# Kernel tuning notes

Measured on AMD Instinct MI355X. Metric: run time of the kernel, lower is better.

The kernel has to match this reference:

```python
import jax, jax.numpy as jnp
import numpy as np

B, S, D = 2, 2048, 1024
H, HD = 16, 64
FF = 4096
LOCAL_W, RAND_P = 256, 0.2
EPS = 1e-5
NEG = -9e15


def _linear_params(key, din, dout):
    kw, kb = jax.random.split(key)
    bound = 1.0 / np.sqrt(din)
    W = jax.random.uniform(kw, (din, dout), jnp.float32, -bound, bound)
    b = jax.random.uniform(kb, (dout,), jnp.float32, -bound, bound)
    return W, b


def setup_inputs() -> dict:
    key = jax.random.key(0)
    ks = jax.random.split(key, 10)
    x = jax.random.normal(ks[0], (B, S, D), jnp.float32)
    # local + random mask, as in create_local_mask
    i = np.arange(S)[:, None]
    j = np.arange(S)[None, :]
    local = (np.abs(i - j) <= LOCAL_W // 2)
    rnd = np.asarray(jax.random.bernoulli(ks[1], RAND_P, (S, S)))
    mask = jnp.asarray(np.logical_or(local, rnd).astype(np.int32))
    Wq, bq = _linear_params(ks[2], D, D)
    Wk, bk = _linear_params(ks[3], D, D)
    Wv, bv = _linear_params(ks[4], D, D)
    Wo, bo = _linear_params(ks[5], D, D)
    W1, b1 = _linear_params(ks[6], D, FF)
    W2, b2 = _linear_params(ks[7], FF, D)
    g1 = jnp.ones((D,), jnp.float32); be1 = jnp.zeros((D,), jnp.float32)
    g2 = jnp.ones((D,), jnp.float32); be2 = jnp.zeros((D,), jnp.float32)
    return dict(x=x, mask=mask, Wq=Wq, bq=bq, Wk=Wk, bk=bk, Wv=Wv, bv=bv,
                Wo=Wo, bo=bo, W1=W1, b1=b1, W2=W2, b2=b2,
                g1=g1, be1=be1, g2=g2, be2=be2)


def _layernorm(x, g, b):
    mu = jnp.mean(x, axis=-1, keepdims=True)
    var = jnp.mean(jnp.square(x - mu), axis=-1, keepdims=True)
    return (x - mu) * jax.lax.rsqrt(var + EPS) * g + b


def reference(x, mask, Wq, bq, Wk, bk, Wv, bv, Wo, bo, W1, b1, W2, b2, g1, be1, g2, be2):
    scale = jnp.float32(np.sqrt(HD))  # sqrt(head_dim), requires_grad=False
    q = x @ Wq + bq
    k = x @ Wk + bk
    v = x @ Wv + bv
    # faithful to original: view(B, heads, S, head_dim) WITHOUT transpose
    q = q.reshape(B, H, S, HD)
    k = k.reshape(B, H, S, HD)
    v = v.reshape(B, H, S, HD)
    scores = jnp.einsum('bhsd,bhtd->bhst', q / scale, k)  # [B,H,S,S]
    scores = jnp.where(mask == 0, jnp.float32(NEG), scores)
    probs = jax.nn.softmax(scores, axis=-1)
    av = jnp.einsum('bhst,bhtd->bhsd', probs, v)
    # faithful reshape back: view(B, S, head_dim*heads)
    attn_out = av.reshape(B, S, H * HD) @ Wo + bo
    x = _layernorm(x + attn_out, g1, be1)
    ffn = jax.nn.gelu(x @ W1 + b1, approximate=False) @ W2 + b2
    x = _layernorm(x + ffn, g2, be2)
    return x
```

## Files before the change

kernel.cpp:

```cpp
#include <hip/hip_runtime.h>
#include <cstdint>
#include <cstddef>

namespace {

constexpr int kS  = 2048;
constexpr int kD  = 1024;
constexpr int kHD = 64;
constexpr int kTOK = 4096;

typedef float f32x4 __attribute__((ext_vector_type(4)));
typedef __bf16 bf16x8 __attribute__((ext_vector_type(8)));
typedef unsigned short u16x8 __attribute__((ext_vector_type(8)));

__device__ __forceinline__ unsigned short f2b(float f){
  unsigned int u = __builtin_bit_cast(unsigned int, f);
  u += 0x7fffu + ((u >> 16) & 1u);
  return (unsigned short)(u >> 16);
}

__device__ __forceinline__ float b2f(unsigned short u){
  return __builtin_bit_cast(float, (unsigned)u << 16);
}

__device__ __forceinline__ bf16x8 ldfrag(const unsigned short* p){
  return __builtin_bit_cast(bf16x8, *(const u16x8*)p);
}

__device__ __forceinline__ float fexp2(float x){
#if __has_builtin(__builtin_amdgcn_exp2f)
  return __builtin_amdgcn_exp2f(x);
#else
  return exp2f(x);
#endif
}

__device__ __forceinline__ void gl_lds16(const void* g, void* l){
  __builtin_amdgcn_global_load_lds(
      (__attribute__((address_space(1))) void*)(void*)g,
      (__attribute__((address_space(3))) void*)l, 16, 0, 0);
}

__device__ __forceinline__ bf16x8 ld_swz(const unsigned short* tile, int row, int slot){
  return ldfrag(tile + row * 64 + (((slot ^ row) & 7) << 3));
}

__device__ __forceinline__ void stageKt(const unsigned short* Kg, unsigned short* lds,
                                        int wave, int lane, int t0){
  #pragma unroll
  for (int i = 0; i < 2; ++i){
    const int lin = i * 4096 + wave * 1024 + lane * 16;
    const int r = lin >> 7;
    const int sl = (lin >> 4) & 7;
    const int sabs = t0 + r;
    gl_lds16(Kg + (size_t)(sabs >> 4) * 3072 + (sabs & 15) * 64 + (((sl ^ r) & 7) << 3),
             (char*)lds + i * 4096 + wave * 1024);
  }
}

__device__ __forceinline__ void stageVt(const unsigned short* Vh, unsigned short* lds,
                                        int wave, int lane, int t0){
  #pragma unroll
  for (int i = 0; i < 2; ++i){
    const int lin = i * 4096 + wave * 1024 + lane * 16;
    const int r = lin >> 7;
    const int sl = (lin >> 4) & 7;
    gl_lds16(Vh + (size_t)r * kS + t0 + (((sl ^ r) & 7) << 3),
             (char*)lds + i * 4096 + wave * 1024);
  }
}

__global__ __launch_bounds__(256) void cvt_bf16_kern(const float* __restrict__ X,
                                                     unsigned short* __restrict__ Y){
  int i = blockIdx.x * 256 + threadIdx.x;
  float4 v = ((const float4*)X)[i];
  ((ushort4*)Y)[i] = make_ushort4(f2b(v.x), f2b(v.y), f2b(v.z), f2b(v.w));
}

__global__ __launch_bounds__(256) void maskbits_kern(const int* __restrict__ mask,
                                                     unsigned long long* __restrict__ mb){
  const int gw   = (blockIdx.x * 256 + threadIdx.x) >> 6;
  const int lane = threadIdx.x & 63;
  const int row  = gw >> 5, word = gw & 31;
  const int key  = ((lane >> 2) & 3) * 16 + ((lane >> 4) & 3) * 4 + (lane & 3);
  const int m = mask[(size_t)row * kS + word * 64 + key];
  const unsigned long long b = __ballot(m != 0);
  if (lane == 0) mb[(size_t)row * 32 + word] = b;
}

__global__ __launch_bounds__(256) void catbias_kern(const float* __restrict__ a,
                                                    const float* __restrict__ b,
                                                    const float* __restrict__ c,
                                                    float* __restrict__ o){
  int i = blockIdx.x * 256 + threadIdx.x;
  float v = (i < 1024) ? a[i] : ((i < 2048) ? b[i - 1024] : c[i - 2048]);
  o[i] = v;
}

__global__ __launch_bounds__(256) void wtrans_kern(const float* __restrict__ W,
                                                   unsigned short* __restrict__ Wt,
                                                   int K, int N){
  __shared__ float t[32][33];
  int n0 = blockIdx.x * 32, k0 = blockIdx.y * 32;
  int tx = threadIdx.x & 31, ty = threadIdx.x >> 5;
  #pragma unroll
  for (int i = 0; i < 32; i += 8)
    t[ty + i][tx] = W[(size_t)(k0 + ty + i) * N + n0 + tx];
  __syncthreads();
  #pragma unroll
  for (int i = 0; i < 32; i += 8)
    Wt[(size_t)(n0 + ty + i) * K + k0 + tx] = f2b(t[tx][ty + i]);
}

__global__ __launch_bounds__(256) void vtrans_kern(const unsigned short* __restrict__ QKV,
                                                   unsigned short* __restrict__ Vt){
  __shared__ unsigned short t[64][65];
  int bh = blockIdx.y, s0 = blockIdx.x * 64;
  const int rowbase = (bh >> 4) * 2048 + (bh & 15) * 128;
  const unsigned short* Vg = QKV + (size_t)rowbase * 3072 + 2048;
  unsigned short* Vth = Vt + (size_t)bh * kHD * kS;
  int tx = threadIdx.x & 63, ty = threadIdx.x >> 6;
  #pragma unroll
  for (int i = 0; i < 64; i += 4){
    const int s = s0 + ty + i;
    t[ty + i][tx] = Vg[(size_t)(s >> 4) * 3072 + (s & 15) * 64 + tx];
  }
  __syncthreads();
  #pragma unroll
  for (int i = 0; i < 64; i += 4)
    Vth[(size_t)(ty + i) * kS + s0 + tx] = t[tx][ty + i];
}

template <int OUT_BF16, int ACT_GELU, int SPLITK>
__global__ __launch_bounds__(512, 2) void gemm256_kern(const unsigned short* __restrict__ A,
                                                       const unsigned short* __restrict__ Bt,
                                                       const float* __restrict__ bias,
                                                       void* __restrict__ C,
                                                       int M, int N, int K){
  __shared__ unsigned short As[2][2][128 * 64];
  __shared__ unsigned short Bs[2][2][128 * 64];
  int bid = blockIdx.y * gridDim.x + blockIdx.x;
  const int nwg = gridDim.x * gridDim.y;
  bid = (bid & 7) * (nwg >> 3) + (bid >> 3);
  const int bx = bid % gridDim.x, by = bid / gridDim.x;
  const int m0 = by << 8, n0 = bx << 8;
  const int tid  = threadIdx.x;
  const int wave = tid >> 6, lane = tid & 63;
  const int wr = wave >> 2, wc = wave & 3;
  const int lr = lane & 15, lk = lane >> 4;
  const int kz   = K / SPLITK;
  const int kbeg = (SPLITK > 1) ? blockIdx.z * kz : 0;
  const int NT   = kz >> 6;
  const int srow = tid >> 3;
  const int scol = ((tid & 7) ^ (srow & 7)) << 3;
  const unsigned short* Ag = A  + (size_t)(m0 + srow) * K + kbeg + scol;
  const unsigned short* Bg = Bt + (size_t)(n0 + srow) * K + kbeg + scol;
  const int dst = tid * 8;
  const int sk0 = ((    lk) ^ (lr & 7)) << 3;
  const int sk1 = ((4 + lk) ^ (lr & 7)) << 3;
  const int aro = lr * 64;
  const int bro = ((wc & 1) * 64 + lr) * 64;
  const int bh_ = wc >> 1;

  f32x4 acc[8][4] = {};
  bf16x8 aR[4][2], bR[2][2][2];

  auto stA = [&](int b, int h, int kt){
    const unsigned short* s = Ag + (size_t)(h * 128) * K + kt * 64;
    gl_lds16(s,                  &As[b][h][dst]);
    gl_lds16(s + (size_t)64 * K, &As[b][h][4096 + dst]);
  };
  auto stB = [&](int b, int h, int kt){
    const unsigned short* s = Bg + (size_t)(h * 128) * K + kt * 64;
    gl_lds16(s,                  &Bs[b][h][dst]);
    gl_lds16(s + (size_t)64 * K, &Bs[b][h][4096 + dst]);
  };

#define LOAD_A(b, MH) { \
  _Pragma("unroll") for (int mp = 0; mp < 4; ++mp){ \
    aR[mp][0] = ldfrag(&As[b][wr][aro + ((MH) * 64 + mp * 16) * 64 + sk0]); \
    aR[mp][1] = ldfrag(&As[b][wr][aro + ((MH) * 64 + mp * 16) * 64 + sk1]); } }
#define LOAD_B(b, NH) { \
  _Pragma("unroll") for (int np = 0; np < 2; ++np){ \
    bR[NH][np][0] = ldfrag(&Bs[b][bh_][bro + ((NH) * 32 + np * 16) * 64 + sk0]); \
    bR[NH][np][1] = ldfrag(&Bs[b][bh_][bro + ((NH) * 32 + np * 16) * 64 + sk1]); } }
#define QMFMA(MH, NH) { \
  _Pragma("unroll") for (int kk = 0; kk < 2; ++kk) \
  _Pragma("unroll") for (int mp = 0; mp < 4; ++mp) \
  _Pragma("unroll") for (int np = 0; np < 2; ++np) \
    acc[(MH)*4+mp][(NH)*2+np] = __builtin_amdgcn_mfma_f32_16x16x32_bf16( \
        aR[mp][kk], bR[NH][np][kk], acc[(MH)*4+mp][(NH)*2+np], 0, 0, 0); }
#define PHASE_TAIL(QM) \
  asm volatile("s_barrier" ::: "memory"); \
  asm volatile("s_waitcnt lgkmcnt(0)" ::: "memory"); \
  __builtin_amdgcn_sched_barrier(0); \
  __builtin_amdgcn_s_setprio(1); \
  QM; \
  __builtin_amdgcn_s_setprio(0); \
  __builtin_amdgcn_sched_barrier(0); \
  asm volatile("s_barrier" ::: "memory");

  stA(0, 0, 0); stB(0, 0, 0); stB(0, 1, 0); stA(0, 1, 0);
  asm volatile("s_waitcnt vmcnt(4)" ::: "memory");
  asm volatile("s_barrier" ::: "memory");

  for (int t = 0; t < NT; ++t){
    const int b = t & 1, bn = b ^ 1;
    const bool pf = (t + 1 < NT);
    LOAD_A(b, 0); LOAD_B(b, 0);
    if (pf){ stA(bn, 0, t + 1); asm volatile("s_waitcnt vmcnt(4)" ::: "memory"); }
    else   {                    asm volatile("s_waitcnt vmcnt(2)" ::: "memory"); }
    PHASE_TAIL(QMFMA(0, 0));
    LOAD_B(b, 1);
    if (pf){ stB(bn, 0, t + 1); asm volatile("s_waitcnt vmcnt(4)" ::: "memory"); }
    else   {                    asm volatile("s_waitcnt vmcnt(0)" ::: "memory"); }
    PHASE_TAIL(QMFMA(0, 1));
    LOAD_A(b, 1);
    if (pf){ stB(bn, 1, t + 1); }
    PHASE_TAIL(QMFMA(1, 0));
    if (pf){ stA(bn, 1, t + 1); asm volatile("s_waitcnt vmcnt(4)" ::: "memory"); }
    PHASE_TAIL(QMFMA(1, 1));
  }
#undef LOAD_A
#undef LOAD_B
#undef QMFMA
#undef PHASE_TAIL

  unsigned short* Cb = (unsigned short*)C + (SPLITK > 1 ? (size_t)blockIdx.z * M * N : 0);
  float*          Cf = (float*)C          + (SPLITK > 1 ? (size_t)blockIdx.z * M * N : 0);
  #pragma unroll
  for (int n = 0; n < 4; ++n){
    const int col = n0 + wc * 64 + n * 16 + lr;
    const float bv = (SPLITK == 1) ? bias[col] : 0.0f;
    #pragma unroll
    for (int m = 0; m < 8; ++m){
      #pragma unroll
      for (int j = 0; j < 4; ++j){
        const int row = m0 + wr * 128 + m * 16 + lk * 4 + j;
        float v = acc[m][n][j] + bv;
        if (ACT_GELU) v = 0.5f * v * (1.0f + erff(v * 0.70710678118654752f));
        if (OUT_BF16) Cb[(size_t)row * N + col] = f2b(v);
        else          Cf[(size_t)row * N + col] = v;
      }
    }
  }
}

__global__ __launch_bounds__(256) void attn_kern(const unsigned short* __restrict__ QKV,
                                                 const unsigned short* __restrict__ Vt,
                                                 const unsigned long long* __restrict__ mbits,
                                                 unsigned short* __restrict__ O){
  __shared__ unsigned short Ks[2][64 * 64];
  __shared__ unsigned short Vs[2][64 * 64];
  __shared__ unsigned short Ps[4][16 * 64];
  const int tid = threadIdx.x;
  const int wave = tid >> 6, lane = tid & 63;
  const int lr = lane & 15, lk = lane >> 4;
  const int bh = blockIdx.y;
  const int rowbase = (bh >> 4) * 2048 + (bh & 15) * 128;
  const unsigned short* Qg = QKV + (size_t)rowbase * 3072;
  const unsigned short* Kg = Qg + 1024;
  const unsigned short* Vh = Vt + (size_t)bh * kHD * kS;
  const int qbase = blockIdx.x * 64 + wave * 16;
  constexpr float kScl = 0.18033688011112042f;

  bf16x8 qf[2];
  { const int qr = qbase + lr;
    const unsigned short* qp = Qg + (size_t)(qr >> 4) * 3072 + (qr & 15) * 64 + lk * 8;
    qf[0] = ldfrag(qp); qf[1] = ldfrag(qp + 32); }

  f32x4 accO[4] = {};
  float lsum = 0.f;
  unsigned short* Pw = Ps[wave];
  char* Pwb = (char*)Pw + lr * 128 + ((lk & 1) << 3);
  const int lr7 = lr & 7;

  const unsigned long long* mrp = mbits + (size_t)(qbase + lr) * 32;
  unsigned long long mb = mrp[0];

  stageKt(Kg, Ks[0], wave, lane, 0);
  stageVt(Vh, Vs[0], wave, lane, 0);
  __syncthreads();

  int cur = 0;
  for (int t = 0; t < kS / 64; ++t){
    unsigned long long mbn = 0;
    if (t < kS / 64 - 1){
      stageKt(Kg, Ks[cur ^ 1], wave, lane, (t + 1) * 64);
      stageVt(Vh, Vs[cur ^ 1], wave, lane, (t + 1) * 64);
      mbn = mrp[t + 1];
    }
    f32x4 sa[4] = {};
    #pragma unroll
    for (int kk = 0; kk < 2; ++kk)
      #pragma unroll
      for (int n = 0; n < 4; ++n){
        bf16x8 kf = ld_swz(Ks[cur], n * 16 + lr, kk * 4 + lk);
        sa[n] = __builtin_amdgcn_mfma_f32_16x16x32_bf16(kf, qf[kk], sa[n], 0, 0, 0);
      }
    const unsigned wb = (unsigned)(mb >> (lk * 16));
    float s = 0.f;
    #pragma unroll
    for (int n = 0; n < 4; ++n){
      float p0, p1, p2, p3;
      {
        float v0 = fexp2(sa[n][0] * kScl), v1 = fexp2(sa[n][1] * kScl);
        float v2 = fexp2(sa[n][2] * kScl), v3 = fexp2(sa[n][3] * kScl);
        const int s0 = ((int)(wb << (31 - (n * 4 + 0)))) >> 31;
        const int s1 = ((int)(wb << (31 - (n * 4 + 1)))) >> 31;
        const int s2 = ((int)(wb << (31 - (n * 4 + 2)))) >> 31;
        const int s3 = ((int)(wb << (31 - (n * 4 + 3)))) >> 31;
        p0 = __builtin_bit_cast(float, __builtin_bit_cast(int, v0) & s0);
        p1 = __builtin_bit_cast(float, __builtin_bit_cast(int, v1) & s1);
        p2 = __builtin_bit_cast(float, __builtin_bit_cast(int, v2) & s2);
        p3 = __builtin_bit_cast(float, __builtin_bit_cast(int, v3) & s3);
      }
      s += (p0 + p1) + (p2 + p3);
      unsigned r0, r1;
      asm("v_cvt_pk_bf16_f32 %0, %1, %2" : "=v"(r0) : "v"(p0), "v"(p1));
      asm("v_cvt_pk_bf16_f32 %0, %1, %2" : "=v"(r1) : "v"(p2), "v"(p3));
      *(uint2*)(Pwb + (((2 * n + (lk >> 1)) ^ lr7) << 4)) = make_uint2(r0, r1);
    }
    s += __shfl_xor(s, 16);
    s += __shfl_xor(s, 32);
    lsum += s;
    #pragma unroll
    for (int kk = 0; kk < 2; ++kk){
      bf16x8 pf = ld_swz(Pw, lr, kk * 4 + lk);
      #pragma unroll
      for (int dd = 0; dd < 4; ++dd){
        bf16x8 vfr = ld_swz(Vs[cur], dd * 16 + lr, kk * 4 + lk);
        accO[dd] = __builtin_amdgcn_mfma_f32_16x16x32_bf16(pf, vfr, accO[dd], 0, 0, 0);
      }
    }
    mb = mbn;
    __syncthreads();
    cur ^= 1;
  }
  const size_t hoff = (size_t)bh * kS * kHD;
  #pragma unroll
  for (int j = 0; j < 4; ++j){
    const float inv = 1.0f / __shfl(lsum, lk * 4 + j);
    const int row = qbase + lk * 4 + j;
    #pragma unroll
    for (int dd = 0; dd < 4; ++dd)
      O[hoff + (size_t)row * 64 + dd * 16 + lr] = f2b(accO[dd][j] * inv);
  }
}

template <int NP, int PBF16, int OUT_B>
__global__ __launch_bounds__(256) void add_ln_kern(const float* __restrict__ X,
                                                   const void* __restrict__ P,
                                                   const float* __restrict__ bias,
                                                   const float* __restrict__ g,
                                                   const float* __restrict__ be,
                                                   float* __restrict__ Yf,
                                                   unsigned short* __restrict__ Yb){
  const int row = blockIdx.x;
  const int tid = threadIdx.x;
  const size_t pstride = (size_t)kTOK * kD;
  const int idx = row * 256 + tid;
  float r0 = 0.f, r1 = 0.f, r2 = 0.f, r3 = 0.f;
  #pragma unroll
  for (int z = 0; z < NP; ++z){
    if (PBF16){
      ushort4 u = ((const ushort4*)P)[z * (pstride / 4) + idx];
      r0 += b2f(u.x); r1 += b2f(u.y); r2 += b2f(u.z); r3 += b2f(u.w);
    } else {
      float4 p = ((const float4*)P)[z * (pstride / 4) + idx];
      r0 += p.x; r1 += p.y; r2 += p.z; r3 += p.w;
    }
  }
  const float4 bb = ((const float4*)bias)[tid];
  const float4 xv = ((const float4*)X)[idx];
  const float a0 = xv.x + r0 + bb.x, a1 = xv.y + r1 + bb.y;
  const float a2 = xv.z + r2 + bb.z, a3 = xv.w + r3 + bb.w;
  float s = a0 + a1 + a2 + a3;
  float q = a0*a0 + a1*a1 + a2*a2 + a3*a3;
  #pragma unroll
  for (int d = 1; d < 64; d <<= 1){ s += __shfl_xor(s, d); q += __shfl_xor(q, d); }
  __shared__ float red[8];
  const int wave = tid >> 6, lane = tid & 63;
  if (lane == 0){ red[wave] = s; red[4 + wave] = q; }
  __syncthreads();
  s = red[0] + red[1] + red[2] + red[3];
  q = red[4] + red[5] + red[6] + red[7];
  const float mu   = s * (1.0f / kD);
  const float var  = q * (1.0f / kD) - mu * mu;
  const float rstd = rsqrtf(var + 1e-5f);
  const float4 gv = ((const float4*)g)[tid];
  const float4 bv = ((const float4*)be)[tid];
  const float y0 = (a0 - mu) * rstd * gv.x + bv.x;
  const float y1 = (a1 - mu) * rstd * gv.y + bv.y;
  const float y2 = (a2 - mu) * rstd * gv.z + bv.z;
  const float y3 = (a3 - mu) * rstd * gv.w + bv.w;
  ((float4*)Yf)[idx] = make_float4(y0, y1, y2, y3);
  if (OUT_B)
    ((ushort4*)Yb)[idx] = make_ushort4(f2b(y0), f2b(y1), f2b(y2), f2b(y3));
}

}

extern "C" void kernel_launch(void* const* d_in, const int* in_sizes, int n_in,
                              void* d_out, int out_size, void* d_ws, size_t ws_size,
                              hipStream_t stream){
  (void)in_sizes; (void)n_in; (void)out_size;
  const float* x   = (const float*)d_in[0];
  const int*   mask= (const int*)d_in[1];
  const float* Wq  = (const float*)d_in[2];  const float* bq  = (const float*)d_in[3];
  const float* Wk  = (const float*)d_in[4];  const float* bk  = (const float*)d_in[5];
  const float* Wv  = (const float*)d_in[6];  const float* bv  = (const float*)d_in[7];
  const float* Wo  = (const float*)d_in[8];  const float* bo  = (const float*)d_in[9];
  const float* W1  = (const float*)d_in[10]; const float* b1  = (const float*)d_in[11];
  const float* W2  = (const float*)d_in[12]; const float* b2  = (const float*)d_in[13];
  const float* g1  = (const float*)d_in[14]; const float* be1 = (const float*)d_in[15];
  const float* g2  = (const float*)d_in[16]; const float* be2 = (const float*)d_in[17];

  char* ws = (char*)d_ws;
  const size_t MB = 1024 * 1024;
  if (ws_size < 96 * MB) return;

  unsigned short* W2T   = (unsigned short*)(ws + 0 * MB);
  unsigned short* W1T   = (unsigned short*)(ws + 8 * MB);
  unsigned short* WqkvT = (unsigned short*)(ws + 16 * MB);
  unsigned short* WoT   = (unsigned short*)(ws + 22 * MB);
  unsigned short* xb    = (unsigned short*)(ws + 24 * MB);
  unsigned short* qkv   = (unsigned short*)(ws + 32 * MB);
  unsigned short* vt    = (unsigned short*)(ws + 56 * MB);
  unsigned short* av    = (unsigned short*)(ws + 64 * MB);
  unsigned long long* mbits = (unsigned long long*)(ws + 72 * MB);
  float* bqkv           = (float*)(ws + 72 * MB + 512 * 1024);
  unsigned short* woP   = (unsigned short*)(ws + 32 * MB);
  float* y32            = (float*)(ws + 72 * MB);
  unsigned short* yb    = (unsigned short*)(ws + 88 * MB);
  unsigned short* hb    = (unsigned short*)(ws + 40 * MB);
  unsigned short* w2p   = (unsigned short*)(ws + 8 * MB);

  dim3 blk(256), gblk(512);
  wtrans_kern<<<dim3(32, 32),  blk, 0, stream>>>(Wq, WqkvT,                   1024, 1024);
  wtrans_kern<<<dim3(32, 32),  blk, 0, stream>>>(Wk, WqkvT + 1024 * 1024,     1024, 1024);
  wtrans_kern<<<dim3(32, 32),  blk, 0, stream>>>(Wv, WqkvT + 2 * 1024 * 1024, 1024, 1024);
  wtrans_kern<<<dim3(32, 32),  blk, 0, stream>>>(Wo, WoT, 1024, 1024);
  wtrans_kern<<<dim3(128, 32), blk, 0, stream>>>(W1, W1T, 1024, 4096);
  wtrans_kern<<<dim3(32, 128), blk, 0, stream>>>(W2, W2T, 4096, 1024);
  cvt_bf16_kern<<<dim3(kTOK * kD / 1024), blk, 0, stream>>>(x, xb);
  maskbits_kern<<<dim3(kS * 32 / 4), blk, 0, stream>>>(mask, mbits);
  catbias_kern<<<dim3(12), blk, 0, stream>>>(bq, bk, bv, bqkv);

  gemm256_kern<1,0,1><<<dim3(12, 16), gblk, 0, stream>>>(xb, WqkvT, bqkv, qkv, 4096, 3072, 1024);

  vtrans_kern<<<dim3(32, 32), blk, 0, stream>>>(qkv, vt);
  attn_kern<<<dim3(32, 32), blk, 0, stream>>>(qkv, vt, mbits, av);

  gemm256_kern<1,0,4><<<dim3(4, 16, 4), gblk, 0, stream>>>(av, WoT, bo, woP, 4096, 1024, 1024);
  add_ln_kern<4,1,1><<<dim3(4096), blk, 0, stream>>>(x, woP, bo, g1, be1, y32, yb);

  gemm256_kern<1,1,1><<<dim3(16, 16), gblk, 0, stream>>>(yb, W1T, b1, hb, 4096, 4096, 1024);
  gemm256_kern<1,0,4><<<dim3(4, 16, 4), gblk, 0, stream>>>(hb, W2T, b2, w2p, 4096, 1024, 4096);
  add_ln_kern<4,1,0><<<dim3(4096), blk, 0, stream>>>(y32, w2p, b2, g2, be2, (float*)d_out, nullptr);
}
```

Baseline: 282.0 us.

## Move softmax scale into QKV GEMM, use halfword mask and MFMA row sums

Folds the attention scale (1/sqrt(d)·log2e) into the QKV GEMM epilogue for the Q columns, which removes the per-score multiply from the attention loop. The packed 64-bit mask bits are replaced by a halfword-expanded mask (0xffff per kept key) that is ANDed directly onto the packed bf16 probabilities. The scalar row-sum with shuffles is replaced by an extra MFMA against a ones vector, so the denominator is now the sum of bf16-rounded probabilities. The cost is a mask buffer 16x larger to read per query tile (4 MB read per attention row sweep instead of 256 KB), plus the Q values are now rounded to bf16 after scaling.

Result: slower. 294.2 us (+4.3%).

```diff
diff --git a/kernel.cpp b/kernel.cpp
--- a/kernel.cpp
+++ b/kernel.cpp
@@ -77,15 +77,11 @@
   ((ushort4*)Y)[i] = make_ushort4(f2b(v.x), f2b(v.y), f2b(v.z), f2b(v.w));
 }
 
-__global__ __launch_bounds__(256) void maskbits_kern(const int* __restrict__ mask,
-                                                     unsigned long long* __restrict__ mb){
-  const int gw   = (blockIdx.x * 256 + threadIdx.x) >> 6;
-  const int lane = threadIdx.x & 63;
-  const int row  = gw >> 5, word = gw & 31;
-  const int key  = ((lane >> 2) & 3) * 16 + ((lane >> 4) & 3) * 4 + (lane & 3);
-  const int m = mask[(size_t)row * kS + word * 64 + key];
-  const unsigned long long b = __ballot(m != 0);
-  if (lane == 0) mb[(size_t)row * 32 + word] = b;
+__global__ __launch_bounds__(256) void mhalf_kern(const int* __restrict__ mask,
+                                                  unsigned* __restrict__ mh){
+  int i = blockIdx.x * 256 + threadIdx.x;
+  const int2 m = ((const int2*)mask)[i];
+  mh[i] = (m.x ? 0x0000ffffu : 0u) | (m.y ? 0xffff0000u : 0u);
 }
 
 __global__ __launch_bounds__(256) void catbias_kern(const float* __restrict__ a,
@@ -131,7 +127,7 @@
     Vth[(size_t)(ty + i) * kS + s0 + tx] = t[tx][ty + i];
 }
 
-template <int OUT_BF16, int ACT_GELU, int SPLITK>
+template <int OUT_BF16, int ACT_GELU, int SPLITK, int SCLQ>
 __global__ __launch_bounds__(512, 2) void gemm256_kern(const unsigned short* __restrict__ A,
                                                        const unsigned short* __restrict__ Bt,
                                                        const float* __restrict__ bias,
@@ -232,6 +228,7 @@
   for (int n = 0; n < 4; ++n){
     const int col = n0 + wc * 64 + n * 16 + lr;
     const float bv = (SPLITK == 1) ? bias[col] : 0.0f;
+    const float cscl = (SCLQ && col < 1024) ? 0.18033688011112042f : 1.0f;
     #pragma unroll
     for (int m = 0; m < 8; ++m){
       #pragma unroll
@@ -239,6 +236,7 @@
         const int row = m0 + wr * 128 + m * 16 + lk * 4 + j;
         float v = acc[m][n][j] + bv;
         if (ACT_GELU) v = 0.5f * v * (1.0f + erff(v * 0.70710678118654752f));
+        if (SCLQ) v *= cscl;
         if (OUT_BF16) Cb[(size_t)row * N + col] = f2b(v);
         else          Cf[(size_t)row * N + col] = v;
       }
@@ -248,7 +246,7 @@
 
 __global__ __launch_bounds__(256) void attn_kern(const unsigned short* __restrict__ QKV,
                                                  const unsigned short* __restrict__ Vt,
-                                                 const unsigned long long* __restrict__ mbits,
+                                                 const unsigned* __restrict__ mh,
                                                  unsigned short* __restrict__ O){
   __shared__ unsigned short Ks[2][64 * 64];
   __shared__ unsigned short Vs[2][64 * 64];
@@ -262,21 +260,24 @@
   const unsigned short* Kg = Qg + 1024;
   const unsigned short* Vh = Vt + (size_t)bh * kHD * kS;
   const int qbase = blockIdx.x * 64 + wave * 16;
-  constexpr float kScl = 0.18033688011112042f;
 
   bf16x8 qf[2];
   { const int qr = qbase + lr;
     const unsigned short* qp = Qg + (size_t)(qr >> 4) * 3072 + (qr & 15) * 64 + lk * 8;
     qf[0] = ldfrag(qp); qf[1] = ldfrag(qp + 32); }
 
+  const bf16x8 onesf = __builtin_bit_cast(bf16x8, (u16x8)((unsigned short)0x3F80));
+
   f32x4 accO[4] = {};
-  float lsum = 0.f;
+  f32x4 accS = {};
   unsigned short* Pw = Ps[wave];
   char* Pwb = (char*)Pw + lr * 128 + ((lk & 1) << 3);
   const int lr7 = lr & 7;
 
-  const unsigned long long* mrp = mbits + (size_t)(qbase + lr) * 32;
-  unsigned long long mb = mrp[0];
+  const unsigned* mhrow = mh + (size_t)(qbase + lr) * (kS / 2) + lk * 2;
+  uint2 mw[4], mwn[4];
+  #pragma unroll
+  for (int n = 0; n < 4; ++n) mw[n] = *(const uint2*)(mhrow + n * 8);
 
   stageKt(Kg, Ks[0], wave, lane, 0);
   stageVt(Vh, Vs[0], wave, lane, 0);
@@ -284,11 +285,11 @@
 
   int cur = 0;
   for (int t = 0; t < kS / 64; ++t){
-    unsigned long long mbn = 0;
     if (t < kS / 64 - 1){
       stageKt(Kg, Ks[cur ^ 1], wave, lane, (t + 1) * 64);
       stageVt(Vh, Vs[cur ^ 1], wave, lane, (t + 1) * 64);
-      mbn = mrp[t + 1];
+      #pragma unroll
+      for (int n = 0; n < 4; ++n) mwn[n] = *(const uint2*)(mhrow + (t + 1) * 32 + n * 8);
     }
     f32x4 sa[4] = {};
     #pragma unroll
@@ -298,49 +299,35 @@
         bf16x8 kf = ld_swz(Ks[cur], n * 16 + lr, kk * 4 + lk);
         sa[n] = __builtin_amdgcn_mfma_f32_16x16x32_bf16(kf, qf[kk], sa[n], 0, 0, 0);
       }
-    const unsigned wb = (unsigned)(mb >> (lk * 16));
-    float s = 0.f;
     #pragma unroll
     for (int n = 0; n < 4; ++n){
-      float p0, p1, p2, p3;
-      {
-        float v0 = fexp2(sa[n][0] * kScl), v1 = fexp2(sa[n][1] * kScl);
-        float v2 = fexp2(sa[n][2] * kScl), v3 = fexp2(sa[n][3] * kScl);
-        const int s0 = ((int)(wb << (31 - (n * 4 + 0)))) >> 31;
-        const int s1 = ((int)(wb << (31 - (n * 4 + 1)))) >> 31;
-        const int s2 = ((int)(wb << (31 - (n * 4 + 2)))) >> 31;
-        const int s3 = ((int)(wb << (31 - (n * 4 + 3)))) >> 31;
-        p0 = __builtin_bit_cast(float, __builtin_bit_cast(int, v0) & s0);
-        p1 = __builtin_bit_cast(float, __builtin_bit_cast(int, v1) & s1);
-        p2 = __builtin_bit_cast(float, __builtin_bit_cast(int, v2) & s2);
-        p3 = __builtin_bit_cast(float, __builtin_bit_cast(int, v3) & s3);
-      }
-      s += (p0 + p1) + (p2 + p3);
+      float p0 = fexp2(sa[n][0]), p1 = fexp2(sa[n][1]);
+      float p2 = fexp2(sa[n][2]), p3 = fexp2(sa[n][3]);
       unsigned r0, r1;
       asm("v_cvt_pk_bf16_f32 %0, %1, %2" : "=v"(r0) : "v"(p0), "v"(p1));
       asm("v_cvt_pk_bf16_f32 %0, %1, %2" : "=v"(r1) : "v"(p2), "v"(p3));
+      r0 &= mw[n].x; r1 &= mw[n].y;
       *(uint2*)(Pwb + (((2 * n + (lk >> 1)) ^ lr7) << 4)) = make_uint2(r0, r1);
     }
-    s += __shfl_xor(s, 16);
-    s += __shfl_xor(s, 32);
-    lsum += s;
     #pragma unroll
     for (int kk = 0; kk < 2; ++kk){
       bf16x8 pf = ld_swz(Pw, lr, kk * 4 + lk);
+      accS = __builtin_amdgcn_mfma_f32_16x16x32_bf16(pf, onesf, accS, 0, 0, 0);
       #pragma unroll
       for (int dd = 0; dd < 4; ++dd){
         bf16x8 vfr = ld_swz(Vs[cur], dd * 16 + lr, kk * 4 + lk);
         accO[dd] = __builtin_amdgcn_mfma_f32_16x16x32_bf16(pf, vfr, accO[dd], 0, 0, 0);
       }
     }
-    mb = mbn;
+    #pragma unroll
+    for (int n = 0; n < 4; ++n) mw[n] = mwn[n];
     __syncthreads();
     cur ^= 1;
   }
   const size_t hoff = (size_t)bh * kS * kHD;
   #pragma unroll
   for (int j = 0; j < 4; ++j){
-    const float inv = 1.0f / __shfl(lsum, lk * 4 + j);
+    const float inv = 1.0f / accS[j];
     const int row = qbase + lk * 4 + j;
     #pragma unroll
     for (int dd = 0; dd < 4; ++dd)
@@ -428,8 +415,8 @@
   unsigned short* qkv   = (unsigned short*)(ws + 32 * MB);
   unsigned short* vt    = (unsigned short*)(ws + 56 * MB);
   unsigned short* av    = (unsigned short*)(ws + 64 * MB);
-  unsigned long long* mbits = (unsigned long long*)(ws + 72 * MB);
-  float* bqkv           = (float*)(ws + 72 * MB + 512 * 1024);
+  unsigned* mh          = (unsigned*)(ws + 72 * MB);
+  float* bqkv           = (float*)(ws + 80 * MB);
   unsigned short* woP   = (unsigned short*)(ws + 32 * MB);
   float* y32            = (float*)(ws + 72 * MB);
   unsigned short* yb    = (unsigned short*)(ws + 88 * MB);
@@ -444,18 +431,18 @@
   wtrans_kern<<<dim3(128, 32), blk, 0, stream>>>(W1, W1T, 1024, 4096);
   wtrans_kern<<<dim3(32, 128), blk, 0, stream>>>(W2, W2T, 4096, 1024);
   cvt_bf16_kern<<<dim3(kTOK * kD / 1024), blk, 0, stream>>>(x, xb);
-  maskbits_kern<<<dim3(kS * 32 / 4), blk, 0, stream>>>(mask, mbits);
+  mhalf_kern<<<dim3(kS * (kS / 2) / 256), blk, 0, stream>>>(mask, mh);
   catbias_kern<<<dim3(12), blk, 0, stream>>>(bq, bk, bv, bqkv);
 
-  gemm256_kern<1,0,1><<<dim3(12, 16), gblk, 0, stream>>>(xb, WqkvT, bqkv, qkv, 4096, 3072, 1024);
+  gemm256_kern<1,0,1,1><<<dim3(12, 16), gblk, 0, stream>>>(xb, WqkvT, bqkv, qkv, 4096, 3072, 1024);
 
   vtrans_kern<<<dim3(32, 32), blk, 0, stream>>>(qkv, vt);
-  attn_kern<<<dim3(32, 32), blk, 0, stream>>>(qkv, vt, mbits, av);
-
-  gemm256_kern<1,0,4><<<dim3(4, 16, 4), gblk, 0, stream>>>(av, WoT, bo, woP, 4096, 1024, 1024);
+  attn_kern<<<dim3(32, 32), blk, 0, stream>>>(qkv, vt, mh, av);
+
+  gemm256_kern<1,0,4,0><<<dim3(4, 16, 4), gblk, 0, stream>>>(av, WoT, bo, woP, 4096, 1024, 1024);
   add_ln_kern<4,1,1><<<dim3(4096), blk, 0, stream>>>(x, woP, bo, g1, be1, y32, yb);
 
-  gemm256_kern<1,1,1><<<dim3(16, 16), gblk, 0, stream>>>(yb, W1T, b1, hb, 4096, 4096, 1024);
-  gemm256_kern<1,0,4><<<dim3(4, 16, 4), gblk, 0, stream>>>(hb, W2T, b2, w2p, 4096, 1024, 4096);
+  gemm256_kern<1,1,1,0><<<dim3(16, 16), gblk, 0, stream>>>(yb, W1T, b1, hb, 4096, 4096, 1024);
+  gemm256_kern<1,0,4,0><<<dim3(4, 16, 4), gblk, 0, stream>>>(hb, W2T, b2, w2p, 4096, 1024, 4096);
   add_ln_kern<4,1,0><<<dim3(4096), blk, 0, stream>>>(y32, w2p, b2, g2, be2, (float*)d_out, nullptr);
 }
```
